# Optimization experiments

Measured on AMD Instinct MI355X. Metric: run time of the kernel, lower is better.

The kernel has to match this reference:

```python
import jax, jax.numpy as jnp
import numpy as np

N = 50000      # nodes
E = 800000     # edges (avg degree 16)
F_IN = 64      # node_features (== GENConv out, so no input projection)
H = 64         # hidden
EXP = 2 * H    # GENConv MLP expansion dim = 128
D2 = F_IN + H  # dense-block concat dim = SAGEConv in = 128
EPS_MSG = 1e-7 # GENConv message eps
BN_EPS = 1e-5


def setup_inputs() -> dict:
    key = jax.random.key(0)
    ks = jax.random.split(key, 16)
    g = lambda k, shape, fan: jax.random.normal(k, shape, jnp.float32) / np.sqrt(fan)
    return {
        "x": jax.random.normal(ks[0], (N, F_IN), jnp.float32),
        "edge_index": jax.random.randint(ks[1], (2, E), 0, N, jnp.int32),
        # GENConv MLP: Linear(64,128) -> BatchNorm(128) -> ReLU -> Linear(128,64)
        "W1": g(ks[2], (H, EXP), H), "b1": jnp.zeros((EXP,), jnp.float32),
        "gamma": jnp.ones((EXP,), jnp.float32), "beta": jnp.zeros((EXP,), jnp.float32),
        "W2": g(ks[3], (EXP, H), EXP), "b2": jnp.zeros((H,), jnp.float32),
        # SAGEConv project Linear(128,128), lin_l Linear(128,64), lin_r Linear(128,64,bias=False)
        "Wp": g(ks[4], (D2, D2), D2), "bp": jnp.zeros((D2,), jnp.float32),
        "Wl": g(ks[5], (D2, H), D2), "bl": jnp.zeros((H,), jnp.float32),
        "Wr": g(ks[6], (D2, H), D2),
        # fc Linear(64,1)
        "Wf": g(ks[7], (H, 1), H), "bf": jnp.zeros((1,), jnp.float32),
    }


def _forward(x, W1, b1, gamma, beta, W2, b2, Wp, bp, Wl, bl, Wr, Wf, bf, src, dst):
    n = x.shape[0]
    # ---- GENConv(aggr='softmax', t=1.0): msg = relu(x_j) + eps -------------
    msg = jax.nn.relu(x[src]) + EPS_MSG                       # [E, H]
    mmax = jax.ops.segment_max(msg, dst, num_segments=n)      # per-dst, per-feature max
    mmax = jax.lax.stop_gradient(jnp.where(jnp.isfinite(mmax), mmax, 0.0))
    e = jnp.exp(msg - mmax[dst])                              # t = 1.0
    denom = jax.ops.segment_sum(e, dst, num_segments=n)
    numer = jax.ops.segment_sum(e * msg, dst, num_segments=n)
    agg = numer / jnp.where(denom > 0, denom, 1.0)            # softmax aggregation
    out = agg + x                                             # residual with x_dst
    # GENConv MLP (BatchNorm in training mode: batch stats, biased var)
    h = out @ W1 + b1
    mu = h.mean(axis=0)
    var = h.var(axis=0)
    h = (h - mu) * jax.lax.rsqrt(var + BN_EPS) * gamma + beta
    h = jax.nn.relu(h) @ W2 + b2                              # [N, H]
    # ---- DeepGCNLayer block='dense': concat input ---------------------------
    x2 = jnp.concatenate([x, h], axis=-1)                     # [N, F_IN+H]
    x2 = jax.nn.sigmoid(x2)                                   # self.relu = Sigmoid()
    # ---- SAGEConv(project=True, aggr=DeepSetsAggregation()==sum) -----------
    xp = jax.nn.relu(x2 @ Wp + bp)                            # projected source feats
    aggr = jax.ops.segment_sum(xp[src], dst, num_segments=n)  # DeepSets w/o nns = sum
    out2 = aggr @ Wl + bl + x2 @ Wr                           # root uses UNprojected x2
    out2 = jax.nn.sigmoid(out2)
    logits = out2 @ Wf + bf                                   # [N, 1]
    probs = jax.nn.sigmoid(logits)                            # training branch
    return probs, logits


def reference(x, edge_index, W1, b1, gamma, beta, W2, b2, Wp, bp, Wl, bl, Wr, Wf, bf):
    src, dst = edge_index[0], edge_index[1]
    return _forward(x, W1, b1, gamma, beta, W2, b2, Wp, bp, Wl, bl, Wr, Wf, bf, src, dst)
```

## Files before the change

### kernel.cpp

```cpp
#include <hip/hip_runtime.h>

#define F_IN 64
#define HID 64
#define EXPD 128
#define D2 128
#define MAXDEG 64
#define NBW 128
#define NB 391
#define BINCAP 2400
#define EPT 32

typedef __attribute__((ext_vector_type(8))) short bf16x8;
typedef __attribute__((ext_vector_type(4))) float f32x4;

__device__ __forceinline__ float sigmoidf_(float x) {
    return 1.0f / (1.0f + __expf(-x));
}
__device__ __forceinline__ unsigned bf16rne_(float f) {
    unsigned u = __float_as_uint(f);
    return (u + 0x7FFFu + ((u >> 16) & 1u)) >> 16;
}
__device__ __forceinline__ float bf16tof_(unsigned u16) {
    return __uint_as_float(u16 << 16);
}

__global__ __launch_bounds__(256) void k_bin(const int* __restrict__ ei,
                                             int* __restrict__ binCount,
                                             unsigned* __restrict__ binned,
                                             const float* __restrict__ x,
                                             unsigned short* __restrict__ x16,
                                             const float* __restrict__ W1,
                                             const float* __restrict__ W2,
                                             const float* __restrict__ Wp,
                                             const float* __restrict__ Wl,
                                             const float* __restrict__ Wr,
                                             short* __restrict__ dst,
                                             int nE, int n, int nbinb) {
    int b = blockIdx.x;
    if (b < nbinb) {
        __shared__ int hist[NB];
        __shared__ int base[NB];
        int tid = threadIdx.x;
        for (int i = tid; i < NB; i += 256) hist[i] = 0;
        __syncthreads();
        unsigned ed[EPT];
        unsigned short rk[EPT];
        int e0 = b * (256 * EPT);
#pragma unroll
        for (int j = 0; j < EPT; ++j) {
            int e = e0 + j * 256 + tid;
            if (e < nE) {
                unsigned s = (unsigned)ei[e];
                unsigned d = (unsigned)ei[nE + e];
                ed[j] = s | (d << 16);
                rk[j] = (unsigned short)atomicAdd(&hist[d >> 7], 1);
            }
        }
        __syncthreads();
        for (int i = tid; i < NB; i += 256) {
            int h = hist[i];
            base[i] = h > 0 ? atomicAdd(&binCount[i], h) : 0;
        }
        __syncthreads();
#pragma unroll
        for (int j = 0; j < EPT; ++j) {
            int e = e0 + j * 256 + tid;
            if (e < nE) {
                int bin = (ed[j] >> 16) >> 7;
                int pos = base[bin] + (int)rk[j];
                if (pos < BINCAP) binned[(size_t)bin * BINCAP + pos] = ed[j];
            }
        }
        return;
    }
    b -= nbinb;
    if (b < 192) {
        int e = b * 256 + threadIdx.x;
        const float* src;
        int K, N, base2;
        if (e < 8192)       { src = W1; K = 64;  N = 128; base2 = 0; }
        else if (e < 16384) { src = W2; K = 128; N = 64;  base2 = 8192; }
        else if (e < 32768) { src = Wp; K = 128; N = 128; base2 = 16384; }
        else if (e < 40960) { src = Wl; K = 128; N = 64;  base2 = 32768; }
        else                { src = Wr; K = 128; N = 64;  base2 = 40960; }
        int le = e - base2;
        int j = le & 7;
        int lane = (le >> 3) & 63;
        int n16 = lane & 15, q = lane >> 4;
        int rest = le >> 9;
        int KC = K / 32;
        int kc = rest % KC, nt = rest / KC;
        int k = kc * 32 + q * 8 + j;
        int col = nt * 16 + n16;
        dst[e] = (short)bf16rne_(src[(size_t)k * N + col]);
        return;
    }
    int i0 = (b - 192) * 1024 + threadIdx.x * 4;
    if (i0 < n * F_IN) {
        float4 v = *(const float4*)(x + i0);
        uint2 pk;
        pk.x = bf16rne_(v.x) | (bf16rne_(v.y) << 16);
        pk.y = bf16rne_(v.z) | (bf16rne_(v.w) << 16);
        *(uint2*)(x16 + i0) = pk;
    }
}

__global__ __launch_bounds__(256) void k_csr(const int* __restrict__ binCount,
                                             const unsigned* __restrict__ binned,
                                             int* __restrict__ counts,
                                             unsigned short* __restrict__ csr, int n) {
    __shared__ unsigned short lcsr[NBW * MAXDEG];
    __shared__ int lcnt[NBW];
    int b = blockIdx.x;
    int tid = threadIdx.x;
    if (tid < NBW) lcnt[tid] = 0;
    __syncthreads();
    int cnt = binCount[b];
    cnt = cnt < BINCAP ? cnt : BINCAP;
    const unsigned* src = binned + (size_t)b * BINCAP;
    for (int i = tid; i < cnt; i += 256) {
        unsigned u = src[i];
        int dl = (int)(u >> 16) - b * NBW;
        int slot = atomicAdd(&lcnt[dl], 1);
        if (slot < MAXDEG) lcsr[dl * MAXDEG + slot] = (unsigned short)(u & 0xFFFF);
    }
    __syncthreads();
    int nodebase = b * NBW;
    if (tid < NBW && nodebase + tid < n) counts[nodebase + tid] = lcnt[tid];
    int nrows = n - nodebase;
    nrows = nrows < NBW ? nrows : NBW;
    int nu4 = nrows * 8;
    uint4* dstrow = (uint4*)(csr + (size_t)nodebase * MAXDEG);
    for (int idx = tid; idx < nu4; idx += 256) dstrow[idx] = ((const uint4*)lcsr)[idx];
}

__global__ __launch_bounds__(256) void k_gen(const unsigned short* __restrict__ x16,
                                             const int* __restrict__ counts,
                                             const unsigned short* __restrict__ csr,
                                             unsigned short* __restrict__ gen16, int n) {
    const unsigned* x32 = (const unsigned*)x16;
    int wid = threadIdx.x >> 6;
    int lane = threadIdx.x & 63;
    int H = lane >> 5, f2 = lane & 31;
    int v = blockIdx.x * 4 + wid;
    if (v >= n) return;
    int deg = counts[v];
    deg = deg > MAXDEG ? MAXDEG : deg;
    int idx = 0;
    if (lane < deg) idx = (int)csr[(size_t)v * MAXDEG + lane];
    float d0 = 0.f, d1 = 0.f, n0 = 0.f, n1 = 0.f;
    int i = 0;
    for (; i + 8 <= deg; i += 8) {
        int sA = __shfl(idx, i + 0 + H, 64);
        int sB = __shfl(idx, i + 2 + H, 64);
        int sC = __shfl(idx, i + 4 + H, 64);
        int sD = __shfl(idx, i + 6 + H, 64);
        unsigned uA = x32[(size_t)sA * 32 + f2];
        unsigned uB = x32[(size_t)sB * 32 + f2];
        unsigned uC = x32[(size_t)sC * 32 + f2];
        unsigned uD = x32[(size_t)sD * 32 + f2];
#pragma unroll
        for (int t = 0; t < 4; ++t) {
            unsigned u = t == 0 ? uA : t == 1 ? uB : t == 2 ? uC : uD;
            float m0 = fmaxf(bf16tof_(u & 0xFFFF), 0.f) + 1e-7f;
            float m1 = fmaxf(bf16tof_(u >> 16), 0.f) + 1e-7f;
            float e0 = __expf(m0), e1 = __expf(m1);
            d0 += e0; d1 += e1;
            n0 = fmaf(e0, m0, n0);
            n1 = fmaf(e1, m1, n1);
        }
    }
    for (; i + 2 <= deg; i += 2) {
        int s = __shfl(idx, i + H, 64);
        unsigned u = x32[(size_t)s * 32 + f2];
        float m0 = fmaxf(bf16tof_(u & 0xFFFF), 0.f) + 1e-7f;
        float m1 = fmaxf(bf16tof_(u >> 16), 0.f) + 1e-7f;
        float e0 = __expf(m0), e1 = __expf(m1);
        d0 += e0; d1 += e1;
        n0 = fmaf(e0, m0, n0);
        n1 = fmaf(e1, m1, n1);
    }
    if (i < deg) {
        int s = __shfl(idx, i, 64);
        if (H == 0) {
            unsigned u = x32[(size_t)s * 32 + f2];
            float m0 = fmaxf(bf16tof_(u & 0xFFFF), 0.f) + 1e-7f;
            float m1 = fmaxf(bf16tof_(u >> 16), 0.f) + 1e-7f;
            float e0 = __expf(m0), e1 = __expf(m1);
            d0 += e0; d1 += e1;
            n0 = fmaf(e0, m0, n0);
            n1 = fmaf(e1, m1, n1);
        }
    }
    d0 += __shfl_xor(d0, 32, 64);
    d1 += __shfl_xor(d1, 32, 64);
    n0 += __shfl_xor(n0, 32, 64);
    n1 += __shfl_xor(n1, 32, 64);
    if (H == 0) {
        float a0 = (deg > 0) ? (n0 / d0) : 0.f;
        float a1 = (deg > 0) ? (n1 / d1) : 0.f;
        unsigned xv = x32[(size_t)v * 32 + f2];
        float r0 = a0 + bf16tof_(xv & 0xFFFF);
        float r1 = a1 + bf16tof_(xv >> 16);
        ((unsigned*)gen16)[(size_t)v * 32 + f2] =
            bf16rne_(r0) | (bf16rne_(r1) << 16);
    }
}

__global__ __launch_bounds__(256) void k_gemm1(const unsigned short* __restrict__ gen16,
                                               const short* __restrict__ Wf,
                                               const float* __restrict__ b1,
                                               unsigned short* __restrict__ h16,
                                               float* __restrict__ bnsums, int n) {
    __shared__ short As[64 * 64];
    __shared__ float bnred[256];
    int tid = threadIdx.x;
    int rblk = blockIdx.x * 64;
    if (tid < 256) bnred[tid] = 0.f;
#pragma unroll
    for (int it = 0; it < 2; ++it) {
        int c = it * 256 + tid;
        int rr = c & 63, q8 = c >> 6;
        int gr = rblk + rr;
        gr = gr < n ? gr : n - 1;
        uint4 v = *(const uint4*)(gen16 + (size_t)gr * F_IN + q8 * 8);
        int slot = ((rr >> 4) * 2 + (q8 >> 2)) * 64 + (q8 & 3) * 16 + (rr & 15);
        *(uint4*)(As + slot * 8) = v;
    }
    __syncthreads();
    int L = tid & 63, w = tid >> 6;
    int q = L >> 4, n16 = L & 15;
    int mt_base = (w & 1) * 2;
    int nt_base = (w >> 1) * 4;
    f32x4 acc[2][4];
#pragma unroll
    for (int mt = 0; mt < 2; ++mt)
#pragma unroll
        for (int nt = 0; nt < 4; ++nt) acc[mt][nt] = (f32x4){0.f, 0.f, 0.f, 0.f};
#pragma unroll
    for (int kc = 0; kc < 2; ++kc) {
        bf16x8 a0 = *(const bf16x8*)(As + (((mt_base + 0) * 2 + kc) * 64 + L) * 8);
        bf16x8 a1 = *(const bf16x8*)(As + (((mt_base + 1) * 2 + kc) * 64 + L) * 8);
#pragma unroll
        for (int nt = 0; nt < 4; ++nt) {
            bf16x8 b = *(const bf16x8*)(Wf + (size_t)(((nt_base + nt) * 2 + kc) * 64 + L) * 8);
            acc[0][nt] = __builtin_amdgcn_mfma_f32_16x16x32_bf16(a0, b, acc[0][nt], 0, 0, 0);
            acc[1][nt] = __builtin_amdgcn_mfma_f32_16x16x32_bf16(a1, b, acc[1][nt], 0, 0, 0);
        }
    }
#pragma unroll
    for (int nt = 0; nt < 4; ++nt) {
        int col = (nt_base + nt) * 16 + n16;
        float bv = b1[col];
        float s = 0.f, s2 = 0.f;
#pragma unroll
        for (int mt = 0; mt < 2; ++mt)
#pragma unroll
            for (int r = 0; r < 4; ++r) {
                int row = rblk + (w & 1) * 32 + mt * 16 + q * 4 + r;
                float hv = acc[mt][nt][r] + bv;
                if (row < n) {
                    h16[(size_t)row * EXPD + col] = (unsigned short)bf16rne_(hv);
                    s += hv;
                    s2 = fmaf(hv, hv, s2);
                }
            }
        s += __shfl_xor(s, 16, 64);
        s += __shfl_xor(s, 32, 64);
        s2 += __shfl_xor(s2, 16, 64);
        s2 += __shfl_xor(s2, 32, 64);
        if (q == 0) {
            atomicAdd(&bnred[col], s);
            atomicAdd(&bnred[128 + col], s2);
        }
    }
    __syncthreads();
    if (tid < 256) atomicAdd(&bnsums[tid], bnred[tid]);
}

__global__ __launch_bounds__(256) void k_mlp2a(const unsigned short* __restrict__ h16,
                                               const float* __restrict__ bnsums,
                                               const float* __restrict__ gamma,
                                               const float* __restrict__ beta,
                                               const short* __restrict__ Wf,
                                               const float* __restrict__ b2,
                                               const unsigned short* __restrict__ x16,
                                               unsigned short* __restrict__ x2_16,
                                               float inv_n, int n) {
    __shared__ short As[128 * 128];
    __shared__ float ssl[256];
    int tid = threadIdx.x;
    int rblk = blockIdx.x * 128;
    if (tid < 128) {
        float mu = bnsums[tid] * inv_n;
        float var = fmaf(-mu, mu, bnsums[128 + tid] * inv_n);
        float rs = rsqrtf(fmaxf(var, 0.f) + 1e-5f);
        float scale = gamma[tid] * rs;
        ssl[tid] = scale;
        ssl[128 + tid] = fmaf(-mu, scale, beta[tid]);
    }
    __syncthreads();
#pragma unroll
    for (int it = 0; it < 8; ++it) {
        int c = it * 256 + tid;
        int rr = c & 127, q8 = c >> 7;
        int gr = rblk + rr;
        gr = gr < n ? gr : n - 1;
        uint4 v = *(const uint4*)(h16 + (size_t)gr * EXPD + q8 * 8);
        float4 sc1 = *(const float4*)(ssl + q8 * 8);
        float4 sc2 = *(const float4*)(ssl + q8 * 8 + 4);
        float4 sh1 = *(const float4*)(ssl + 128 + q8 * 8);
        float4 sh2 = *(const float4*)(ssl + 128 + q8 * 8 + 4);
        float o0 = fmaxf(fmaf(bf16tof_(v.x & 0xFFFF), sc1.x, sh1.x), 0.f);
        float o1 = fmaxf(fmaf(bf16tof_(v.x >> 16),    sc1.y, sh1.y), 0.f);
        float o2 = fmaxf(fmaf(bf16tof_(v.y & 0xFFFF), sc1.z, sh1.z), 0.f);
        float o3 = fmaxf(fmaf(bf16tof_(v.y >> 16),    sc1.w, sh1.w), 0.f);
        float o4 = fmaxf(fmaf(bf16tof_(v.z & 0xFFFF), sc2.x, sh2.x), 0.f);
        float o5 = fmaxf(fmaf(bf16tof_(v.z >> 16),    sc2.y, sh2.y), 0.f);
        float o6 = fmaxf(fmaf(bf16tof_(v.w & 0xFFFF), sc2.z, sh2.z), 0.f);
        float o7 = fmaxf(fmaf(bf16tof_(v.w >> 16),    sc2.w, sh2.w), 0.f);
        uint4 pk;
        pk.x = bf16rne_(o0) | (bf16rne_(o1) << 16);
        pk.y = bf16rne_(o2) | (bf16rne_(o3) << 16);
        pk.z = bf16rne_(o4) | (bf16rne_(o5) << 16);
        pk.w = bf16rne_(o6) | (bf16rne_(o7) << 16);
        int slot = ((rr >> 4) * 4 + (q8 >> 2)) * 64 + (q8 & 3) * 16 + (rr & 15);
        *(uint4*)(As + slot * 8) = pk;
    }
    __syncthreads();
    int L = tid & 63, w = tid >> 6;
    int q = L >> 4, n16 = L & 15;
    int mt_base = w * 2;
    f32x4 acc[2][4];
#pragma unroll
    for (int mt = 0; mt < 2; ++mt)
#pragma unroll
        for (int nt = 0; nt < 4; ++nt) acc[mt][nt] = (f32x4){0.f, 0.f, 0.f, 0.f};
#pragma unroll
    for (int kc = 0; kc < 4; ++kc) {
        bf16x8 a0 = *(const bf16x8*)(As + (((mt_base + 0) * 4 + kc) * 64 + L) * 8);
        bf16x8 a1 = *(const bf16x8*)(As + (((mt_base + 1) * 4 + kc) * 64 + L) * 8);
#pragma unroll
        for (int nt = 0; nt < 4; ++nt) {
            bf16x8 b = *(const bf16x8*)(Wf + (size_t)((nt * 4 + kc) * 64 + L) * 8);
            acc[0][nt] = __builtin_amdgcn_mfma_f32_16x16x32_bf16(a0, b, acc[0][nt], 0, 0, 0);
            acc[1][nt] = __builtin_amdgcn_mfma_f32_16x16x32_bf16(a1, b, acc[1][nt], 0, 0, 0);
        }
    }
#pragma unroll
    for (int it = 0; it < 8; ++it) {
        int i = it * 256 + tid;
        int rr = i >> 4, c4 = i & 15;
        int row = rblk + rr;
        if (row < n) {
            uint2 xv = ((const uint2*)x16)[(size_t)row * 16 + c4];
            float s0 = sigmoidf_(bf16tof_(xv.x & 0xFFFF));
            float s1 = sigmoidf_(bf16tof_(xv.x >> 16));
            float s2 = sigmoidf_(bf16tof_(xv.y & 0xFFFF));
            float s3 = sigmoidf_(bf16tof_(xv.y >> 16));
            uint2 pk;
            pk.x = bf16rne_(s0) | (bf16rne_(s1) << 16);
            pk.y = bf16rne_(s2) | (bf16rne_(s3) << 16);
            *(uint2*)(x2_16 + (size_t)row * D2 + c4 * 4) = pk;
        }
    }
#pragma unroll
    for (int nt = 0; nt < 4; ++nt) {
        int col = nt * 16 + n16;
        float bv = b2[col];
#pragma unroll
        for (int mt = 0; mt < 2; ++mt)
#pragma unroll
            for (int r = 0; r < 4; ++r) {
                int row = rblk + w * 32 + mt * 16 + q * 4 + r;
                if (row < n)
                    x2_16[(size_t)row * D2 + 64 + col] =
                        (unsigned short)bf16rne_(sigmoidf_(acc[mt][nt][r] + bv));
            }
    }
}

__global__ __launch_bounds__(256) void k_mlp2b(const unsigned short* __restrict__ x2_16,
                                               const short* __restrict__ Wfp,
                                               const short* __restrict__ Wfl,
                                               const float* __restrict__ bp,
                                               unsigned short* __restrict__ yp16, int n) {
    __shared__ short As[64 * 128];
    int tid = threadIdx.x;
    int rblk = blockIdx.x * 64;
#pragma unroll
    for (int it = 0; it < 4; ++it) {
        int c = it * 256 + tid;
        int rr = c & 63, q8 = c >> 6;
        int gr = rblk + rr;
        gr = gr < n ? gr : n - 1;
        uint4 v = *(const uint4*)(x2_16 + (size_t)gr * D2 + q8 * 8);
        int slot = ((rr >> 4) * 4 + (q8 >> 2)) * 64 + (q8 & 3) * 16 + (rr & 15);
        *(uint4*)(As + slot * 8) = v;
    }
    __syncthreads();
    int L = tid & 63, w = tid >> 6;
    int q = L >> 4, n16 = L & 15;
    int mt_base = (w & 1) * 2;
    int nt_base = (w >> 1) * 4;
    f32x4 acc[2][4];
#pragma unroll
    for (int mt = 0; mt < 2; ++mt)
#pragma unroll
        for (int nt = 0; nt < 4; ++nt) acc[mt][nt] = (f32x4){0.f, 0.f, 0.f, 0.f};
#pragma unroll
    for (int kc = 0; kc < 4; ++kc) {
        bf16x8 a0 = *(const bf16x8*)(As + (((mt_base + 0) * 4 + kc) * 64 + L) * 8);
        bf16x8 a1 = *(const bf16x8*)(As + (((mt_base + 1) * 4 + kc) * 64 + L) * 8);
#pragma unroll
        for (int nt = 0; nt < 4; ++nt) {
            bf16x8 b = *(const bf16x8*)(Wfp + (size_t)(((nt_base + nt) * 4 + kc) * 64 + L) * 8);
            acc[0][nt] = __builtin_amdgcn_mfma_f32_16x16x32_bf16(a0, b, acc[0][nt], 0, 0, 0);
            acc[1][nt] = __builtin_amdgcn_mfma_f32_16x16x32_bf16(a1, b, acc[1][nt], 0, 0, 0);
        }
    }
    __syncthreads();
#pragma unroll
    for (int nt = 0; nt < 4; ++nt) {
        int kk = (nt_base + nt) * 16 + n16;
        float bv = bp[kk];
        int q8b = kk >> 3, jb = kk & 7;
#pragma unroll
        for (int mt = 0; mt < 2; ++mt)
#pragma unroll
            for (int r = 0; r < 4; ++r) {
                int rr2 = (w & 1) * 32 + mt * 16 + q * 4 + r;
                float xv = fmaxf(acc[mt][nt][r] + bv, 0.f);
                int slot = ((rr2 >> 4) * 4 + (q8b >> 2)) * 64 + (q8b & 3) * 16 + (rr2 & 15);
                As[slot * 8 + jb] = (short)bf16rne_(xv);
            }
    }
    __syncthreads();
    f32x4 acc2[4];
#pragma unroll
    for (int nt = 0; nt < 4; ++nt) acc2[nt] = (f32x4){0.f, 0.f, 0.f, 0.f};
#pragma unroll
    for (int kc = 0; kc < 4; ++kc) {
        bf16x8 a = *(const bf16x8*)(As + ((w * 4 + kc) * 64 + L) * 8);
#pragma unroll
        for (int nt = 0; nt < 4; ++nt) {
            bf16x8 b = *(const bf16x8*)(Wfl + (size_t)((nt * 4 + kc) * 64 + L) * 8);
            acc2[nt] = __builtin_amdgcn_mfma_f32_16x16x32_bf16(a, b, acc2[nt], 0, 0, 0);
        }
    }
#pragma unroll
    for (int nt = 0; nt < 4; ++nt) {
        int col = nt * 16 + n16;
#pragma unroll
        for (int r = 0; r < 4; ++r) {
            int row = rblk + w * 16 + q * 4 + r;
            if (row < n)
                yp16[(size_t)row * HID + col] = (unsigned short)bf16rne_(acc2[nt][r]);
        }
    }
}

__global__ __launch_bounds__(256) void k_sage(const unsigned short* __restrict__ yp16,
                                              const int* __restrict__ counts,
                                              const unsigned short* __restrict__ csr,
                                              unsigned short* __restrict__ aggr16, int n) {
    const unsigned* yp32 = (const unsigned*)yp16;
    int wid = threadIdx.x >> 6;
    int lane = threadIdx.x & 63;
    int H = lane >> 5, f2 = lane & 31;
    int v = blockIdx.x * 4 + wid;
    if (v >= n) return;
    int deg = counts[v];
    deg = deg > MAXDEG ? MAXDEG : deg;
    int idx = 0;
    if (lane < deg) idx = (int)csr[(size_t)v * MAXDEG + lane];
    float a0 = 0.f, a1 = 0.f;
    int i = 0;
    for (; i + 8 <= deg; i += 8) {
        int sA = __shfl(idx, i + 0 + H, 64);
        int sB = __shfl(idx, i + 2 + H, 64);
        int sC = __shfl(idx, i + 4 + H, 64);
        int sD = __shfl(idx, i + 6 + H, 64);
        unsigned uA = yp32[(size_t)sA * 32 + f2];
        unsigned uB = yp32[(size_t)sB * 32 + f2];
        unsigned uC = yp32[(size_t)sC * 32 + f2];
        unsigned uD = yp32[(size_t)sD * 32 + f2];
        a0 += bf16tof_(uA & 0xFFFF) + bf16tof_(uB & 0xFFFF) +
              bf16tof_(uC & 0xFFFF) + bf16tof_(uD & 0xFFFF);
        a1 += bf16tof_(uA >> 16) + bf16tof_(uB >> 16) +
              bf16tof_(uC >> 16) + bf16tof_(uD >> 16);
    }
    for (; i + 2 <= deg; i += 2) {
        int s = __shfl(idx, i + H, 64);
        unsigned u = yp32[(size_t)s * 32 + f2];
        a0 += bf16tof_(u & 0xFFFF);
        a1 += bf16tof_(u >> 16);
    }
    if (i < deg) {
        int s = __shfl(idx, i, 64);
        if (H == 0) {
            unsigned u = yp32[(size_t)s * 32 + f2];
            a0 += bf16tof_(u & 0xFFFF);
            a1 += bf16tof_(u >> 16);
        }
    }
    a0 += __shfl_xor(a0, 32, 64);
    a1 += __shfl_xor(a1, 32, 64);
    if (H == 0)
        ((unsigned*)aggr16)[(size_t)v * 32 + f2] = bf16rne_(a0) | (bf16rne_(a1) << 16);
}

__global__ __launch_bounds__(256) void k_final(const unsigned short* __restrict__ aggr16,
                                               const unsigned short* __restrict__ x2_16,
                                               const short* __restrict__ Wfr,
                                               const float* __restrict__ bl,
                                               const float* __restrict__ Wfv,
                                               const float* __restrict__ bf,
                                               float* __restrict__ out, int n) {
    __shared__ short As[128 * 128];
    int tid = threadIdx.x;
    int rblk = blockIdx.x * 128;
#pragma unroll
    for (int it = 0; it < 8; ++it) {
        int c = it * 256 + tid;
        int rr = c & 127, q8 = c >> 7;
        int gr = rblk + rr;
        gr = gr < n ? gr : n - 1;
        uint4 v = *(const uint4*)(x2_16 + (size_t)gr * D2 + q8 * 8);
        int slot = ((rr >> 4) * 4 + (q8 >> 2)) * 64 + (q8 & 3) * 16 + (rr & 15);
        *(uint4*)(As + slot * 8) = v;
    }
    __syncthreads();
    int L = tid & 63, w = tid >> 6;
    int q = L >> 4, n16 = L & 15;
    int mt_base = w * 2;
    f32x4 acc[2][4];
#pragma unroll
    for (int mt = 0; mt < 2; ++mt)
#pragma unroll
        for (int nt = 0; nt < 4; ++nt) acc[mt][nt] = (f32x4){0.f, 0.f, 0.f, 0.f};
#pragma unroll
    for (int kc = 0; kc < 4; ++kc) {
        bf16x8 a0 = *(const bf16x8*)(As + (((mt_base + 0) * 4 + kc) * 64 + L) * 8);
        bf16x8 a1 = *(const bf16x8*)(As + (((mt_base + 1) * 4 + kc) * 64 + L) * 8);
#pragma unroll
        for (int nt = 0; nt < 4; ++nt) {
            bf16x8 b = *(const bf16x8*)(Wfr + (size_t)((nt * 4 + kc) * 64 + L) * 8);
            acc[0][nt] = __builtin_amdgcn_mfma_f32_16x16x32_bf16(a0, b, acc[0][nt], 0, 0, 0);
            acc[1][nt] = __builtin_amdgcn_mfma_f32_16x16x32_bf16(a1, b, acc[1][nt], 0, 0, 0);
        }
    }
    float blv[4], wfv[4];
#pragma unroll
    for (int nt = 0; nt < 4; ++nt) {
        blv[nt] = bl[nt * 16 + n16];
        wfv[nt] = Wfv[nt * 16 + n16];
    }
    float bf0 = bf[0];
#pragma unroll
    for (int mt = 0; mt < 2; ++mt)
#pragma unroll
        for (int r = 0; r < 4; ++r) {
            int row = rblk + w * 32 + mt * 16 + q * 4 + r;
            int rowc = row < n ? row : n - 1;
            float t = 0.f;
#pragma unroll
            for (int nt = 0; nt < 4; ++nt) {
                float ag = bf16tof_(aggr16[(size_t)rowc * HID + nt * 16 + n16]);
                t = fmaf(sigmoidf_(acc[mt][nt][r] + blv[nt] + ag), wfv[nt], t);
            }
            t += __shfl_xor(t, 1, 64);
            t += __shfl_xor(t, 2, 64);
            t += __shfl_xor(t, 4, 64);
            t += __shfl_xor(t, 8, 64);
            if (n16 == 0 && row < n) {
                float lg = t + bf0;
                out[row] = sigmoidf_(lg);
                out[n + row] = lg;
            }
        }
}

extern "C" void kernel_launch(void* const* d_in, const int* in_sizes, int n_in,
                              void* d_out, int out_size, void* d_ws, size_t ws_size,
                              hipStream_t stream) {
    const float* x     = (const float*)d_in[0];
    const int*   ei    = (const int*)d_in[1];
    const float* W1    = (const float*)d_in[2];
    const float* b1    = (const float*)d_in[3];
    const float* gamma = (const float*)d_in[4];
    const float* beta  = (const float*)d_in[5];
    const float* W2    = (const float*)d_in[6];
    const float* b2    = (const float*)d_in[7];
    const float* Wp    = (const float*)d_in[8];
    const float* bp    = (const float*)d_in[9];
    const float* Wl    = (const float*)d_in[10];
    const float* bl    = (const float*)d_in[11];
    const float* Wr    = (const float*)d_in[12];
    const float* Wfv   = (const float*)d_in[13];
    const float* bf    = (const float*)d_in[14];
    const int n = in_sizes[0] / F_IN;
    const int e = in_sizes[1] / 2;

    char* ws = (char*)d_ws;
    size_t off = 0;
    auto alloc = [&](size_t bytes) -> void* {
        void* p = (void*)(ws + off);
        off += (bytes + 255) & ~(size_t)255;
        return p;
    };
    float*          bnsums   = (float*)alloc(256 * 4 + NB * 4);
    int*            binCount = (int*)((char*)bnsums + 1024);
    int*            counts   = (int*)alloc((size_t)n * 4);
    unsigned short* csr      = (unsigned short*)alloc((size_t)n * MAXDEG * 2);
    unsigned*       binned   = (unsigned*)alloc((size_t)NB * BINCAP * 4);
    unsigned short* x16      = (unsigned short*)alloc((size_t)n * F_IN * 2);
    unsigned short* gen16    = (unsigned short*)alloc((size_t)n * F_IN * 2);
    unsigned short* h16      = (unsigned short*)alloc((size_t)n * EXPD * 2);
    unsigned short* x2_16    = (unsigned short*)alloc((size_t)n * D2 * 2);
    unsigned short* yp16     = (unsigned short*)alloc((size_t)n * HID * 2);
    unsigned short* aggr16   = (unsigned short*)alloc((size_t)n * HID * 2);
    short*          wfrag    = (short*)alloc(49152 * 2);

    float* out = (float*)d_out;
    const int nb64  = (n + 63) / 64;
    const int nb128 = (n + 127) / 128;
    const int nb4   = (n + 3) / 4;
    const int nbinb = (e + 256 * EPT - 1) / (256 * EPT);
    const int nfp = nbinb + 192 + ((n * F_IN + 1023) / 1024);

    hipMemsetAsync(bnsums, 0, 1024 + NB * 4, stream);

    k_bin<<<nfp, 256, 0, stream>>>(ei, binCount, binned, x, x16, W1, W2, Wp, Wl,
                                   Wr, wfrag, e, n, nbinb);
    k_csr<<<NB, 256, 0, stream>>>(binCount, binned, counts, csr, n);
    k_gen<<<nb4, 256, 0, stream>>>(x16, counts, csr, gen16, n);
    k_gemm1<<<nb64, 256, 0, stream>>>(gen16, wfrag, b1, h16, bnsums, n);
    k_mlp2a<<<nb128, 256, 0, stream>>>(h16, bnsums, gamma, beta, wfrag + 8192, b2,
                                       x16, x2_16, 1.0f / (float)n, n);
    k_mlp2b<<<nb64, 256, 0, stream>>>(x2_16, wfrag + 16384, wfrag + 32768, bp,
                                      yp16, n);
    k_sage<<<nb4, 256, 0, stream>>>(yp16, counts, csr, aggr16, n);
    k_final<<<nb128, 256, 0, stream>>>(aggr16, x2_16, wfrag + 40960, bl, Wfv, bf,
                                       out, n);
}
```

Before: 232.9 us.

## Fuse root projection into mlp2b and final epilogue into SAGE aggregation kernel

The x2@Wr root projection now runs inside k_mlp2b, reusing the x2 tile already staged in shared memory, and is written out as a bf16 yr16 buffer. The SAGE aggregation kernel then applies bias, sigmoid, the fc dot product and the output sigmoid directly, so the separate k_final kernel and the aggr16 intermediate go away. This saves one launch and the re-read of x2 (128 features per node), at the cost of an extra yr16 write/read and a second bf16 rounding of the root term.

```diff
diff --git a/kernel.cpp b/kernel.cpp
--- a/kernel.cpp
+++ b/kernel.cpp
@@ -383,8 +383,10 @@
 __global__ __launch_bounds__(256) void k_mlp2b(const unsigned short* __restrict__ x2_16,
                                                const short* __restrict__ Wfp,
                                                const short* __restrict__ Wfl,
+                                               const short* __restrict__ Wfr,
                                                const float* __restrict__ bp,
-                                               unsigned short* __restrict__ yp16, int n) {
+                                               unsigned short* __restrict__ yp16,
+                                               unsigned short* __restrict__ yr16, int n) {
     __shared__ short As[64 * 128];
     int tid = threadIdx.x;
     int rblk = blockIdx.x * 64;
@@ -404,10 +406,14 @@
     int mt_base = (w & 1) * 2;
     int nt_base = (w >> 1) * 4;
     f32x4 acc[2][4];
-#pragma unroll
-    for (int mt = 0; mt < 2; ++mt)
+    f32x4 accr[2][2];
+#pragma unroll
+    for (int mt = 0; mt < 2; ++mt) {
 #pragma unroll
         for (int nt = 0; nt < 4; ++nt) acc[mt][nt] = (f32x4){0.f, 0.f, 0.f, 0.f};
+#pragma unroll
+        for (int nt = 0; nt < 2; ++nt) accr[mt][nt] = (f32x4){0.f, 0.f, 0.f, 0.f};
+    }
 #pragma unroll
     for (int kc = 0; kc < 4; ++kc) {
         bf16x8 a0 = *(const bf16x8*)(As + (((mt_base + 0) * 4 + kc) * 64 + L) * 8);
@@ -418,6 +424,24 @@
             acc[0][nt] = __builtin_amdgcn_mfma_f32_16x16x32_bf16(a0, b, acc[0][nt], 0, 0, 0);
             acc[1][nt] = __builtin_amdgcn_mfma_f32_16x16x32_bf16(a1, b, acc[1][nt], 0, 0, 0);
         }
+#pragma unroll
+        for (int nt = 0; nt < 2; ++nt) {
+            bf16x8 b = *(const bf16x8*)(Wfr + (size_t)((((w >> 1) * 2 + nt) * 4 + kc) * 64 + L) * 8);
+            accr[0][nt] = __builtin_amdgcn_mfma_f32_16x16x32_bf16(a0, b, accr[0][nt], 0, 0, 0);
+            accr[1][nt] = __builtin_amdgcn_mfma_f32_16x16x32_bf16(a1, b, accr[1][nt], 0, 0, 0);
+        }
+    }
+#pragma unroll
+    for (int nt = 0; nt < 2; ++nt) {
+        int col = ((w >> 1) * 2 + nt) * 16 + n16;
+#pragma unroll
+        for (int mt = 0; mt < 2; ++mt)
+#pragma unroll
+            for (int r = 0; r < 4; ++r) {
+                int row = rblk + (w & 1) * 32 + mt * 16 + q * 4 + r;
+                if (row < n)
+                    yr16[(size_t)row * HID + col] = (unsigned short)bf16rne_(accr[mt][nt][r]);
+            }
     }
     __syncthreads();
 #pragma unroll
@@ -460,10 +484,14 @@
     }
 }
 
-__global__ __launch_bounds__(256) void k_sage(const unsigned short* __restrict__ yp16,
-                                              const int* __restrict__ counts,
-                                              const unsigned short* __restrict__ csr,
-                                              unsigned short* __restrict__ aggr16, int n) {
+__global__ __launch_bounds__(256) void k_sagef(const unsigned short* __restrict__ yp16,
+                                               const int* __restrict__ counts,
+                                               const unsigned short* __restrict__ csr,
+                                               const unsigned short* __restrict__ yr16,
+                                               const float* __restrict__ bl,
+                                               const float* __restrict__ Wfv,
+                                               const float* __restrict__ bf,
+                                               float* __restrict__ out, int n) {
     const unsigned* yp32 = (const unsigned*)yp16;
     int wid = threadIdx.x >> 6;
     int lane = threadIdx.x & 63;
@@ -506,79 +534,24 @@
     }
     a0 += __shfl_xor(a0, 32, 64);
     a1 += __shfl_xor(a1, 32, 64);
-    if (H == 0)
-        ((unsigned*)aggr16)[(size_t)v * 32 + f2] = bf16rne_(a0) | (bf16rne_(a1) << 16);
-}
-
-__global__ __launch_bounds__(256) void k_final(const unsigned short* __restrict__ aggr16,
-                                               const unsigned short* __restrict__ x2_16,
-                                               const short* __restrict__ Wfr,
-                                               const float* __restrict__ bl,
-                                               const float* __restrict__ Wfv,
-                                               const float* __restrict__ bf,
-                                               float* __restrict__ out, int n) {
-    __shared__ short As[128 * 128];
-    int tid = threadIdx.x;
-    int rblk = blockIdx.x * 128;
-#pragma unroll
-    for (int it = 0; it < 8; ++it) {
-        int c = it * 256 + tid;
-        int rr = c & 127, q8 = c >> 7;
-        int gr = rblk + rr;
-        gr = gr < n ? gr : n - 1;
-        uint4 v = *(const uint4*)(x2_16 + (size_t)gr * D2 + q8 * 8);
-        int slot = ((rr >> 4) * 4 + (q8 >> 2)) * 64 + (q8 & 3) * 16 + (rr & 15);
-        *(uint4*)(As + slot * 8) = v;
-    }
-    __syncthreads();
-    int L = tid & 63, w = tid >> 6;
-    int q = L >> 4, n16 = L & 15;
-    int mt_base = w * 2;
-    f32x4 acc[2][4];
-#pragma unroll
-    for (int mt = 0; mt < 2; ++mt)
-#pragma unroll
-        for (int nt = 0; nt < 4; ++nt) acc[mt][nt] = (f32x4){0.f, 0.f, 0.f, 0.f};
-#pragma unroll
-    for (int kc = 0; kc < 4; ++kc) {
-        bf16x8 a0 = *(const bf16x8*)(As + (((mt_base + 0) * 4 + kc) * 64 + L) * 8);
-        bf16x8 a1 = *(const bf16x8*)(As + (((mt_base + 1) * 4 + kc) * 64 + L) * 8);
-#pragma unroll
-        for (int nt = 0; nt < 4; ++nt) {
-            bf16x8 b = *(const bf16x8*)(Wfr + (size_t)((nt * 4 + kc) * 64 + L) * 8);
-            acc[0][nt] = __builtin_amdgcn_mfma_f32_16x16x32_bf16(a0, b, acc[0][nt], 0, 0, 0);
-            acc[1][nt] = __builtin_amdgcn_mfma_f32_16x16x32_bf16(a1, b, acc[1][nt], 0, 0, 0);
-        }
-    }
-    float blv[4], wfv[4];
-#pragma unroll
-    for (int nt = 0; nt < 4; ++nt) {
-        blv[nt] = bl[nt * 16 + n16];
-        wfv[nt] = Wfv[nt * 16 + n16];
-    }
-    float bf0 = bf[0];
-#pragma unroll
-    for (int mt = 0; mt < 2; ++mt)
-#pragma unroll
-        for (int r = 0; r < 4; ++r) {
-            int row = rblk + w * 32 + mt * 16 + q * 4 + r;
-            int rowc = row < n ? row : n - 1;
-            float t = 0.f;
-#pragma unroll
-            for (int nt = 0; nt < 4; ++nt) {
-                float ag = bf16tof_(aggr16[(size_t)rowc * HID + nt * 16 + n16]);
-                t = fmaf(sigmoidf_(acc[mt][nt][r] + blv[nt] + ag), wfv[nt], t);
-            }
-            t += __shfl_xor(t, 1, 64);
-            t += __shfl_xor(t, 2, 64);
-            t += __shfl_xor(t, 4, 64);
-            t += __shfl_xor(t, 8, 64);
-            if (n16 == 0 && row < n) {
-                float lg = t + bf0;
-                out[row] = sigmoidf_(lg);
-                out[n + row] = lg;
-            }
-        }
+    if (H == 0) {
+        unsigned u = ((const unsigned*)yr16)[(size_t)v * 32 + f2];
+        float2 blv = ((const float2*)bl)[f2];
+        float2 wv  = ((const float2*)Wfv)[f2];
+        float o0 = sigmoidf_(a0 + blv.x + bf16tof_(u & 0xFFFF));
+        float o1 = sigmoidf_(a1 + blv.y + bf16tof_(u >> 16));
+        float t = fmaf(o0, wv.x, o1 * wv.y);
+        t += __shfl_xor(t, 1, 64);
+        t += __shfl_xor(t, 2, 64);
+        t += __shfl_xor(t, 4, 64);
+        t += __shfl_xor(t, 8, 64);
+        t += __shfl_xor(t, 16, 64);
+        if (f2 == 0) {
+            float lg = t + bf[0];
+            out[v] = sigmoidf_(lg);
+            out[n + v] = lg;
+        }
+    }
 }
 
 extern "C" void kernel_launch(void* const* d_in, const int* in_sizes, int n_in,
@@ -619,7 +592,7 @@
     unsigned short* h16      = (unsigned short*)alloc((size_t)n * EXPD * 2);
     unsigned short* x2_16    = (unsigned short*)alloc((size_t)n * D2 * 2);
     unsigned short* yp16     = (unsigned short*)alloc((size_t)n * HID * 2);
-    unsigned short* aggr16   = (unsigned short*)alloc((size_t)n * HID * 2);
+    unsigned short* yr16     = (unsigned short*)alloc((size_t)n * HID * 2);
     short*          wfrag    = (short*)alloc(49152 * 2);
 
     float* out = (float*)d_out;
@@ -638,9 +611,7 @@
     k_gemm1<<<nb64, 256, 0, stream>>>(gen16, wfrag, b1, h16, bnsums, n);
     k_mlp2a<<<nb128, 256, 0, stream>>>(h16, bnsums, gamma, beta, wfrag + 8192, b2,
                                        x16, x2_16, 1.0f / (float)n, n);
-    k_mlp2b<<<nb64, 256, 0, stream>>>(x2_16, wfrag + 16384, wfrag + 32768, bp,
-                                      yp16, n);
-    k_sage<<<nb4, 256, 0, stream>>>(yp16, counts, csr, aggr16, n);
-    k_final<<<nb128, 256, 0, stream>>>(aggr16, x2_16, wfrag + 40960, bl, Wfv, bf,
-                                       out, n);
-}
+    k_mlp2b<<<nb64, 256, 0, stream>>>(x2_16, wfrag + 16384, wfrag + 32768,
+                                      wfrag + 40960, bp, yp16, yr16, n);
+    k_sagef<<<nb4, 256, 0, stream>>>(yp16, counts, csr, yr16, bl, Wfv, bf, out, n);
+}
```

Measured after the change: 228.9 us. No clear change (-1.7%).
